# Kernel tuning notes

Measured on AMD Instinct MI355X. Metric: run time of the kernel, lower is better.

Reference implementation:

```python
import jax, jax.numpy as jnp
import numpy as np

N_NODES = 50000
N_EDGES = 800000
IN_F = 128
HID = 256
N_CLS = 10
NUM_GRAPHS = 256


def setup_inputs() -> dict:
    key = jax.random.key(0)
    ks = jax.random.split(key, 8)
    x = jax.random.normal(ks[0], (N_NODES, IN_F), dtype=jnp.float32)
    edge_index = jax.random.randint(ks[1], (2, N_EDGES), 0, N_NODES, dtype=jnp.int64)
    batch = jnp.sort(jax.random.randint(ks[2], (N_NODES,), 0, NUM_GRAPHS, dtype=jnp.int64))
    # Glorot-style init for weights (GCNConv default), zeros bias
    W1 = jax.random.normal(ks[3], (IN_F, HID), dtype=jnp.float32) / np.sqrt(IN_F)
    b1 = jnp.zeros((HID,), dtype=jnp.float32)
    W2 = jax.random.normal(ks[4], (HID, HID), dtype=jnp.float32) / np.sqrt(HID)
    b2 = jnp.zeros((HID,), dtype=jnp.float32)
    Wlin = jax.random.normal(ks[5], (HID, N_CLS), dtype=jnp.float32) / np.sqrt(HID)
    blin = jnp.zeros((N_CLS,), dtype=jnp.float32)
    return {"x": x, "edge_index": edge_index, "batch": batch,
            "W1": W1, "b1": b1, "W2": W2, "b2": b2, "Wlin": Wlin, "blin": blin}


def reference(x, edge_index, batch, W1, b1, W2, b2, Wlin, blin):
    N = x.shape[0]
    # PyG GCNConv default: add self-loops, symmetric normalization D^-1/2 A D^-1/2
    loop = jnp.arange(N, dtype=edge_index.dtype)
    src = jnp.concatenate([edge_index[0], loop])  # message source (row)
    dst = jnp.concatenate([edge_index[1], loop])  # aggregation target (col)
    deg = jax.ops.segment_sum(jnp.ones_like(dst, dtype=x.dtype), dst, num_segments=N)
    dinv = jnp.where(deg > 0, jax.lax.rsqrt(deg), 0.0)
    norm = dinv[src] * dinv[dst]  # [E+N]

    def gcn_conv(h, W, b):
        h = h @ W                          # linear transform first (GCNConv)
        msg = h[src] * norm[:, None]       # gather + edge scale
        agg = jax.ops.segment_sum(msg, dst, num_segments=N)  # scatter-add
        return agg + b

    h = jax.nn.relu(gcn_conv(x, W1, b1))
    h = gcn_conv(h, W2, b2)

    # global_mean_pool over batch ids
    counts = jax.ops.segment_sum(jnp.ones((N,), x.dtype), batch, num_segments=NUM_GRAPHS)
    pooled = jax.ops.segment_sum(h, batch, num_segments=NUM_GRAPHS)
    pooled = pooled / jnp.maximum(counts, 1.0)[:, None]  # [NUM_GRAPHS, HID]

    return pooled @ Wlin + blin  # forward returns logits (softmax unused in forward)
```

## Files before the change

### kernel.cpp

```cpp
#include <hip/hip_runtime.h>
#include <hip/hip_bf16.h>

typedef __hip_bfloat16 bf16;
typedef __attribute__((ext_vector_type(8))) short short8;
typedef __attribute__((ext_vector_type(4))) float f32x4;
typedef __attribute__((ext_vector_type(2))) float f32x2;

#define N_NODES 50000
#define N_EDGES 800000
#define IN_F    128
#define HID     256
#define N_CLS   10
#define N_GRAPH 256

#define NB 98
#define PBLOCKS 256

__device__ __forceinline__ int IG(const int* __restrict__ p, int i, int w) {
    return w ? p[2 * i] : p[i];
}
__device__ __forceinline__ float LF(const void* __restrict__ p, int i, int isbf) {
    return isbf ? __bfloat162float(((const bf16*)p)[i]) : ((const float*)p)[i];
}
__device__ __forceinline__ float b2f(unsigned short h) {
    union { unsigned u; float f; } c; c.u = ((unsigned)h) << 16; return c.f;
}
__device__ __forceinline__ unsigned short f2b(float x) {
    bf16 h = __float2bfloat16(x);
    union { bf16 b; unsigned short u; } c; c.b = h; return c.u;
}
__device__ __forceinline__ float f8s(unsigned b) {
    union { unsigned u; float f; } c;
    c.u = ((b & 0x80u) << 24) | ((b & 0x7Fu) << 20);
    return c.f;
}
#define F8SCALE 0x1p120f
__device__ __forceinline__ unsigned f2fp8(float x) {
    unsigned short h = f2b(x * 0x1p-120f);
    unsigned s = ((unsigned)h >> 8) & 0x80u;
    unsigned mag = (unsigned)h & 0x7FFFu;
    unsigned r = (mag + 7u + ((mag >> 4) & 1u)) >> 4;
    if (r > 0x7Eu) r = 0x7Eu;
    return s | r;
}

#if defined(__has_builtin)
#if __has_builtin(__builtin_amdgcn_cvt_pk_f32_fp8)
#define HW_FP8 1
#endif
#if __has_builtin(__builtin_amdgcn_cvt_pk_fp8_f32)
#define HW_FP8E 1
#endif
#endif

__device__ __forceinline__ f32x2 cvt2lo(unsigned v) {
#ifdef HW_FP8
    return __builtin_amdgcn_cvt_pk_f32_fp8((int)v, false);
#else
    f32x2 r; r[0] = f8s(v & 0xFF) * F8SCALE; r[1] = f8s((v >> 8) & 0xFF) * F8SCALE; return r;
#endif
}
__device__ __forceinline__ f32x2 cvt2hi(unsigned v) {
#ifdef HW_FP8
    return __builtin_amdgcn_cvt_pk_f32_fp8((int)v, true);
#else
    f32x2 r; r[0] = f8s((v >> 16) & 0xFF) * F8SCALE; r[1] = f8s(v >> 24) * F8SCALE; return r;
#endif
}
__device__ __forceinline__ unsigned pk4_fp8(float v0, float v1, float v2, float v3) {
#ifdef HW_FP8E
    int o = __builtin_amdgcn_cvt_pk_fp8_f32(v0, v1, 0, false);
    o = __builtin_amdgcn_cvt_pk_fp8_f32(v2, v3, o, true);
    return (unsigned)o;
#else
    return f2fp8(v0) | (f2fp8(v1) << 8) | (f2fp8(v2) << 16) | (f2fp8(v3) << 24);
#endif
}

__global__ __launch_bounds__(256) void k_detect(const int* __restrict__ ei,
                                                const unsigned short* __restrict__ x,
                                                int* __restrict__ flags) {
    __shared__ int nz, cnt;
    if (threadIdx.x == 0) { nz = 0; cnt = 0; }
    __syncthreads();
    int found = 0, c = 0;
    for (int s = 0; s < 4; ++s) {
        int idx = 2 * (threadIdx.x * 4 + s) + 1;
        if (ei[idx] != 0) found = 1;
    }
    for (int s = 0; s < 8; ++s) {
        unsigned short h = x[threadIdx.x * 8 + s];
        int e = (h >> 7) & 0xFF;
        if (e >= 110 && e <= 135) c++;
    }
    if (found) atomicAdd(&nz, 1);
    atomicAdd(&cnt, c);
    __syncthreads();
    if (threadIdx.x == 0) {
        flags[0] = (nz == 0) ? 1 : 0;
        flags[1] = (cnt > 1536) ? 1 : 0;
    }
}

__global__ __launch_bounds__(256) void k_partA1(const int* __restrict__ ei, int* __restrict__ bucketCnt,
                                                int* __restrict__ blockBase, const int* __restrict__ flags,
                                                int E, int N) {
    __shared__ int h[NB];
    int t = threadIdx.x;
    if (t < NB) h[t] = 0;
    __syncthreads();
    int w = flags[0];
    for (int e = blockIdx.x * 256 + t; e < E; e += PBLOCKS * 256) {
        int d = IG(ei, E + e, w);
        int s = IG(ei, e, w);
        if ((unsigned)d < (unsigned)N && (unsigned)s < (unsigned)N)
            atomicAdd(&h[d >> 9], 1);
    }
    __syncthreads();
    if (t < NB)
        blockBase[blockIdx.x * NB + t] = atomicAdd(&bucketCnt[t * 16], h[t]);
}

__global__ __launch_bounds__(128) void k_bscan(const int* __restrict__ bucketCnt,
                                               int* __restrict__ bucketBase) {
    __shared__ int s[128];
    int t = threadIdx.x;
    int v = (t < NB) ? bucketCnt[t * 16] : 0;
    s[t] = v;
    __syncthreads();
    for (int off = 1; off < 128; off <<= 1) {
        int add = (t >= off) ? s[t - off] : 0;
        __syncthreads();
        s[t] += add;
        __syncthreads();
    }
    if (t <= NB) bucketBase[t] = (t < NB) ? (s[t] - v) : s[NB - 1] + 0;
    if (t == NB - 1) bucketBase[NB] = s[t];
}

__global__ __launch_bounds__(256) void k_partA2(const int* __restrict__ ei,
                                                const int* __restrict__ bucketBase,
                                                const int* __restrict__ blockBase,
                                                unsigned* __restrict__ part,
                                                const int* __restrict__ flags, int E, int N) {
    __shared__ int cur[NB];
    int t = threadIdx.x;
    if (t < NB) cur[t] = bucketBase[t] + blockBase[blockIdx.x * NB + t];
    __syncthreads();
    int w = flags[0];
    for (int e = blockIdx.x * 256 + t; e < E; e += PBLOCKS * 256) {
        int d = IG(ei, E + e, w);
        int s = IG(ei, e, w);
        if ((unsigned)d < (unsigned)N && (unsigned)s < (unsigned)N) {
            int slot = atomicAdd(&cur[d >> 9], 1);
            part[slot] = ((unsigned)(d & 511) << 16) | (unsigned)s;
        }
    }
}

__global__ __launch_bounds__(256) void k_partB(const unsigned* __restrict__ part,
                                               const int* __restrict__ bucketBase,
                                               int* __restrict__ rowptr, float* __restrict__ dinv,
                                               int* __restrict__ col, int N) {
    __shared__ int hist[512];
    __shared__ int scn[512];
    __shared__ int pair[256];
    int b = blockIdx.x, t = threadIdx.x;
    int s0 = bucketBase[b], e0 = bucketBase[b + 1];
    hist[t] = 0; hist[t + 256] = 0;
    __syncthreads();
    for (int j = s0 + t; j < e0; j += 256)
        atomicAdd(&hist[part[j] >> 16], 1);
    __syncthreads();
    int a0 = hist[2 * t], a1 = hist[2 * t + 1];
    int pv = a0 + a1;
    pair[t] = pv;
    __syncthreads();
    for (int off = 1; off < 256; off <<= 1) {
        int add = (t >= off) ? pair[t - off] : 0;
        __syncthreads();
        pair[t] += add;
        __syncthreads();
    }
    int pbase = pair[t] - pv;
    scn[2 * t] = pbase;
    scn[2 * t + 1] = pbase + a0;
    __syncthreads();
#pragma unroll
    for (int hh = 0; hh < 2; ++hh) {
        int l = t + hh * 256;
        int node = b * 512 + l;
        if (node < N) {
            rowptr[node] = s0 + scn[l];
            dinv[node] = rsqrtf((float)(hist[l] + 1));
        }
    }
    if (b == 0 && t == 0) rowptr[N] = bucketBase[NB];
    __syncthreads();
    for (int j = s0 + t; j < e0; j += 256) {
        unsigned p = part[j];
        int pos = s0 + atomicAdd(&scn[p >> 16], 1);
        col[pos] = (int)(p & 0xFFFFu);
    }
}

#define CVTX_BLOCKS 6250
#define CVT1_BLOCKS 128
#define CVT2_BLOCKS 256
#define GB_BLOCKS   196
__global__ __launch_bounds__(256) void k_cvt(const void* __restrict__ x, const float* __restrict__ dinv,
                                             unsigned char* __restrict__ xs8,
                                             const void* __restrict__ W1, unsigned short* __restrict__ w1t,
                                             const void* __restrict__ W2, unsigned short* __restrict__ w2t,
                                             const int* __restrict__ batch, int* __restrict__ gstart,
                                             const int* __restrict__ flags) {
    int b = blockIdx.x;
    int fb = flags[1];
    if (b < CVTX_BLOCKS) {
        int gid = b * 256 + threadIdx.x;
        int row = gid >> 5;
        float d = dinv[row];
        float vx, vy, vz, vw;
        if (fb) {
            ushort4 v = ((const ushort4*)x)[gid];
            vx = b2f(v.x); vy = b2f(v.y); vz = b2f(v.z); vw = b2f(v.w);
        } else {
            float4 v = ((const float4*)x)[gid];
            vx = v.x; vy = v.y; vz = v.z; vw = v.w;
        }
        ((unsigned*)xs8)[gid] = pk4_fp8(vx * d, vy * d, vz * d, vw * d);
    } else if (b < CVTX_BLOCKS + CVT1_BLOCKS) {
        int i = (b - CVTX_BLOCKS) * 256 + threadIdx.x;
        int n = i >> 7, k = i & 127;
        w1t[i] = f2b(LF(W1, k * 256 + n, fb));
    } else if (b < CVTX_BLOCKS + CVT1_BLOCKS + CVT2_BLOCKS) {
        int i = (b - CVTX_BLOCKS - CVT1_BLOCKS) * 256 + threadIdx.x;
        int n = i >> 8, k = i & 255;
        w2t[i] = f2b(LF(W2, k * 256 + n, fb));
    } else {
        int i = (b - CVTX_BLOCKS - CVT1_BLOCKS - CVT2_BLOCKS) * 256 + threadIdx.x;
        if (i <= N_NODES) {
            int w = flags[0];
            int prev = (i == 0) ? -1 : IG(batch, i - 1, w);
            int cur  = (i == N_NODES) ? N_GRAPH : IG(batch, i, w);
            if (prev < -1) prev = -1;
            if (cur > N_GRAPH) cur = N_GRAPH;
            for (int g = prev + 1; g <= cur; ++g)
                if (g >= 0 && g <= N_GRAPH) gstart[g] = i;
        }
    }
}

__global__ __launch_bounds__(256) void k_gemm(const unsigned short* __restrict__ A,
                                              const unsigned short* __restrict__ Bt,
                                              unsigned short* __restrict__ C,
                                              unsigned char* __restrict__ C8, int M, int K,
                                              const float* __restrict__ rowscale,
                                              const void* __restrict__ bias,
                                              const int* __restrict__ flags, int relu) {
    __shared__ unsigned char lds[64 * 132 * 4];
    int t = threadIdx.x;
    int lane = t & 63;
    int w = t >> 6;
    int bm = blockIdx.x * 64;
    int l15 = lane & 15, quad = lane >> 4;

    f32x4 acc[4][4];
#pragma unroll
    for (int ar = 0; ar < 4; ++ar)
#pragma unroll
        for (int tt = 0; tt < 4; ++tt) acc[ar][tt] = (f32x4){0.f, 0.f, 0.f, 0.f};

    const unsigned short* ap[4];
    const unsigned short* bp[4];
#pragma unroll
    for (int ar = 0; ar < 4; ++ar)
        ap[ar] = &A[(size_t)(bm + ar * 16 + l15) * K + quad * 8];
#pragma unroll
    for (int tt = 0; tt < 4; ++tt)
        bp[tt] = &Bt[(size_t)(w * 64 + tt * 16 + l15) * K + quad * 8];

    int nks = K >> 5;
    short8 a[4], b[4];
#pragma unroll
    for (int ar = 0; ar < 4; ++ar) a[ar] = *(const short8*)(ap[ar]);
#pragma unroll
    for (int tt = 0; tt < 4; ++tt) b[tt] = *(const short8*)(bp[tt]);
    for (int ks = 0; ks < nks; ++ks) {
        short8 an[4], bn[4];
        int nxt = (ks + 1) * 32;
        if (ks + 1 < nks) {
#pragma unroll
            for (int ar = 0; ar < 4; ++ar) an[ar] = *(const short8*)(ap[ar] + nxt);
#pragma unroll
            for (int tt = 0; tt < 4; ++tt) bn[tt] = *(const short8*)(bp[tt] + nxt);
        }
#pragma unroll
        for (int ar = 0; ar < 4; ++ar)
#pragma unroll
            for (int tt = 0; tt < 4; ++tt)
                acc[ar][tt] = __builtin_amdgcn_mfma_f32_16x16x32_bf16(b[tt], a[ar], acc[ar][tt], 0, 0, 0);
        if (ks + 1 < nks) {
#pragma unroll
            for (int ar = 0; ar < 4; ++ar) a[ar] = an[ar];
#pragma unroll
            for (int tt = 0; tt < 4; ++tt) b[tt] = bn[tt];
        }
    }

    int fb = flags[1];
    float drow[4];
#pragma unroll
    for (int ar = 0; ar < 4; ++ar) {
        int row = bm + ar * 16 + l15;
        drow[ar] = (rowscale && row < M) ? rowscale[row] : 1.f;
    }
    if (C8) {
        unsigned* Cs = (unsigned*)lds;
#pragma unroll
        for (int tt = 0; tt < 4; ++tt) {
            int colb = w * 64 + tt * 16 + quad * 4;
            float bc[4];
#pragma unroll
            for (int rr = 0; rr < 4; ++rr)
                bc[rr] = bias ? LF(bias, colb + rr, fb) : 0.f;
#pragma unroll
            for (int ar = 0; ar < 4; ++ar) {
                float v[4];
#pragma unroll
                for (int rr = 0; rr < 4; ++rr) {
                    float u = fmaf(acc[ar][tt][rr], drow[ar], bc[rr]);
                    v[rr] = relu ? fmaxf(u, 0.f) : u;
                }
                Cs[(ar * 16 + l15) * 68 + w * 16 + tt * 4 + quad] =
                    pk4_fp8(v[0], v[1], v[2], v[3]);
            }
        }
        __syncthreads();
        int r = t >> 2, h = t & 3;
        if (bm + r < M) {
            const unsigned* src = Cs + r * 68 + h * 16;
            uint4* dst = (uint4*)&C8[(size_t)(bm + r) * 256 + h * 64];
#pragma unroll
            for (int j = 0; j < 4; ++j) dst[j] = *(const uint4*)(src + j * 4);
        }
    } else {
        unsigned short* Cs = (unsigned short*)lds;
#pragma unroll
        for (int tt = 0; tt < 4; ++tt) {
            int colb = w * 64 + tt * 16 + quad * 4;
            float bc[4];
#pragma unroll
            for (int rr = 0; rr < 4; ++rr)
                bc[rr] = bias ? LF(bias, colb + rr, fb) : 0.f;
#pragma unroll
            for (int ar = 0; ar < 4; ++ar) {
                float v[4];
#pragma unroll
                for (int rr = 0; rr < 4; ++rr) {
                    float u = fmaf(acc[ar][tt][rr], drow[ar], bc[rr]);
                    v[rr] = relu ? fmaxf(u, 0.f) : u;
                }
                ushort4 o;
                o.x = f2b(v[0]); o.y = f2b(v[1]); o.z = f2b(v[2]); o.w = f2b(v[3]);
                *(ushort4*)&Cs[(ar * 16 + l15) * 264 + w * 64 + tt * 16 + quad * 4] = o;
            }
        }
        __syncthreads();
        int r = t >> 2, h = t & 3;
        if (bm + r < M) {
            int base = r * 264 + h * 64;
            size_t g = (size_t)(bm + r) * 256 + h * 64;
#pragma unroll
            for (int j = 0; j < 8; ++j)
                *(uint4*)&C[g + j * 8] = *(const uint4*)&Cs[base + j * 8];
        }
    }
}

__global__ __launch_bounds__(256) void k_agg2(const unsigned char* __restrict__ XS,
                                              const int* __restrict__ rowptr, const int* __restrict__ col,
                                              unsigned short* __restrict__ Hout, int N) {
    int lane = threadIdx.x & 63;
    int i = (blockIdx.x * 256 + threadIdx.x) >> 6;
    if (i >= N) return;
    int fo = lane * 2;
    unsigned sv = *(const unsigned short*)&XS[(size_t)i * 128 + fo];
    f32x2 a = cvt2lo(sv);
    int s = rowptr[i], e = rowptr[i + 1];
    int j = s;
    while (j + 16 <= e) {
        unsigned v[16];
#pragma unroll
        for (int q = 0; q < 16; ++q)
            v[q] = *(const unsigned short*)&XS[(size_t)col[j + q] * 128 + fo];
#pragma unroll
        for (int q = 0; q < 16; ++q) a += cvt2lo(v[q]);
        j += 16;
    }
    if (j + 8 <= e) {
        unsigned v[8];
#pragma unroll
        for (int q = 0; q < 8; ++q)
            v[q] = *(const unsigned short*)&XS[(size_t)col[j + q] * 128 + fo];
#pragma unroll
        for (int q = 0; q < 8; ++q) a += cvt2lo(v[q]);
        j += 8;
    }
    if (j + 4 <= e) {
        unsigned v[4];
#pragma unroll
        for (int q = 0; q < 4; ++q)
            v[q] = *(const unsigned short*)&XS[(size_t)col[j + q] * 128 + fo];
#pragma unroll
        for (int q = 0; q < 4; ++q) a += cvt2lo(v[q]);
        j += 4;
    }
    for (; j < e; ++j)
        a += cvt2lo(*(const unsigned short*)&XS[(size_t)col[j] * 128 + fo]);
    ushort2 o;
    o.x = f2b(a[0]); o.y = f2b(a[1]);
    *(ushort2*)&Hout[(size_t)i * 128 + fo] = o;
}

__global__ __launch_bounds__(256) void k_agg4(const unsigned char* __restrict__ XW,
                                              const int* __restrict__ rowptr, const int* __restrict__ col,
                                              const float* __restrict__ dinv, const void* __restrict__ bias,
                                              const int* __restrict__ flags,
                                              unsigned short* __restrict__ Hout, int N) {
    int lane = threadIdx.x & 63;
    int i = (blockIdx.x * 256 + threadIdx.x) >> 6;
    if (i >= N) return;
    int fo = lane * 4;
    unsigned sv = *(const unsigned*)&XW[(size_t)i * 256 + fo];
    f32x2 a01 = cvt2lo(sv), a23 = cvt2hi(sv);
    int s = rowptr[i], e = rowptr[i + 1];
    int j = s;
    while (j + 16 <= e) {
        unsigned v[16];
#pragma unroll
        for (int q = 0; q < 16; ++q)
            v[q] = *(const unsigned*)&XW[(size_t)col[j + q] * 256 + fo];
#pragma unroll
        for (int q = 0; q < 16; ++q) { a01 += cvt2lo(v[q]); a23 += cvt2hi(v[q]); }
        j += 16;
    }
    if (j + 8 <= e) {
        unsigned v[8];
#pragma unroll
        for (int q = 0; q < 8; ++q)
            v[q] = *(const unsigned*)&XW[(size_t)col[j + q] * 256 + fo];
#pragma unroll
        for (int q = 0; q < 8; ++q) { a01 += cvt2lo(v[q]); a23 += cvt2hi(v[q]); }
        j += 8;
    }
    if (j + 4 <= e) {
        unsigned v[4];
#pragma unroll
        for (int q = 0; q < 4; ++q)
            v[q] = *(const unsigned*)&XW[(size_t)col[j + q] * 256 + fo];
#pragma unroll
        for (int q = 0; q < 4; ++q) { a01 += cvt2lo(v[q]); a23 += cvt2hi(v[q]); }
        j += 4;
    }
    for (; j < e; ++j) {
        unsigned v = *(const unsigned*)&XW[(size_t)col[j] * 256 + fo];
        a01 += cvt2lo(v); a23 += cvt2hi(v);
    }
    int fb = flags[1];
    float di = dinv[i];
    float bx = LF(bias, fo + 0, fb), by = LF(bias, fo + 1, fb);
    float bz = LF(bias, fo + 2, fb), bw = LF(bias, fo + 3, fb);
    ushort4 o;
    o.x = f2b(fmaf(a01[0], di, bx)); o.y = f2b(fmaf(a01[1], di, by));
    o.z = f2b(fmaf(a23[0], di, bz)); o.w = f2b(fmaf(a23[1], di, bw));
    *(ushort4*)&Hout[(size_t)i * 256 + fo] = o;
}

__global__ __launch_bounds__(256) void k_poolfinal(const unsigned short* __restrict__ H2,
                                                   const int* __restrict__ gstart,
                                                   const void* __restrict__ Wlin,
                                                   const void* __restrict__ blin,
                                                   const int* __restrict__ flags,
                                                   void* __restrict__ outv) {
    __shared__ float red[4][256];
    __shared__ float p[256];
    int g = blockIdx.x, t = threadIdx.x;
    int sub = t >> 6, lane = t & 63;
    int s = gstart[g], e = gstart[g + 1];
    int cnt = e - s;
    float ax = 0.f, ay = 0.f, az = 0.f, aw = 0.f;
    for (int i = s + sub; i < e; i += 4) {
        ushort4 v = *(const ushort4*)&H2[(size_t)i * 256 + lane * 4];
        ax += b2f(v.x); ay += b2f(v.y); az += b2f(v.z); aw += b2f(v.w);
    }
    red[sub][lane * 4 + 0] = ax;
    red[sub][lane * 4 + 1] = ay;
    red[sub][lane * 4 + 2] = az;
    red[sub][lane * 4 + 3] = aw;
    __syncthreads();
    float inv = 1.f / fmaxf((float)cnt, 1.f);
    p[t] = (red[0][t] + red[1][t] + red[2][t] + red[3][t]) * inv;
    __syncthreads();
    int fb = flags[1];
    if (t < N_CLS) {
        float sum = LF(blin, t, fb);
        for (int f = 0; f < HID; ++f) sum = fmaf(p[f], LF(Wlin, f * N_CLS + t, fb), sum);
        if (fb) ((bf16*)outv)[g * N_CLS + t] = __float2bfloat16(sum);
        else    ((float*)outv)[g * N_CLS + t] = sum;
    }
}

extern "C" void kernel_launch(void* const* d_in, const int* in_sizes, int n_in,
                              void* d_out, int out_size, void* d_ws, size_t ws_size,
                              hipStream_t stream) {
    (void)n_in; (void)ws_size; (void)in_sizes; (void)out_size;
    const void* x     = d_in[0];
    const int*  ei    = (const int*)d_in[1];
    const int*  batch = (const int*)d_in[2];
    const void* W1    = d_in[3];
    const void* b1    = d_in[4];
    const void* W2    = d_in[5];
    const void* b2    = d_in[6];
    const void* Wl    = d_in[7];
    const void* bl    = d_in[8];

    const int N = N_NODES, E = N_EDGES, F = IN_F, H = HID, G = N_GRAPH;

    char* ws = (char*)d_ws;
    size_t off = 0;
    auto alloc = [&](size_t bytes) -> void* {
        void* p = ws + off;
        off += (bytes + 511) & ~(size_t)511;
        return p;
    };
    unsigned char*  xs8  = (unsigned char*)alloc((size_t)N * F);
    unsigned short* aggX = (unsigned short*)alloc((size_t)N * F * 2);
    unsigned short* H1   = (unsigned short*)alloc((size_t)N * H * 2);
    unsigned short* H2   = (unsigned short*)alloc((size_t)N * H * 2);
    unsigned char*  XW2s8 = xs8;
    unsigned short* w1t  = (unsigned short*)alloc((size_t)H * F * 2);
    unsigned short* w2t  = (unsigned short*)alloc((size_t)H * H * 2);
    int*   bucketCnt = (int*)alloc((size_t)NB * 16 * 4);
    int*   bucketBase = (int*)alloc((size_t)(NB + 1) * 4);
    int*   blockBase = (int*)alloc((size_t)PBLOCKS * NB * 4);
    unsigned* part  = (unsigned*)alloc((size_t)E * 4);
    int*   gstart  = (int*)alloc((size_t)(G + 1) * 4);
    float* dinv    = (float*)alloc((size_t)N * 4);
    int*   rowptr  = (int*)alloc((size_t)(N + 1) * 4);
    int*   flags   = (int*)alloc(512);
    int*   col     = (int*)alloc((size_t)E * 4);
    size_t zero_bytes = (size_t)NB * 16 * 4;

    hipMemsetAsync(bucketCnt, 0, zero_bytes, stream);

    k_detect<<<1, 256, 0, stream>>>(ei, (const unsigned short*)x, flags);
    k_partA1<<<PBLOCKS, 256, 0, stream>>>(ei, bucketCnt, blockBase, flags, E, N);
    k_bscan<<<1, 128, 0, stream>>>(bucketCnt, bucketBase);
    k_partA2<<<PBLOCKS, 256, 0, stream>>>(ei, bucketBase, blockBase, part, flags, E, N);
    k_partB<<<NB, 256, 0, stream>>>(part, bucketBase, rowptr, dinv, col, N);

    k_cvt<<<CVTX_BLOCKS + CVT1_BLOCKS + CVT2_BLOCKS + GB_BLOCKS, 256, 0, stream>>>(
        x, dinv, xs8, W1, w1t, W2, w2t, batch, gstart, flags);

    int gemmBlocks = (N + 63) / 64;
    int nbAgg = (N + 3) / 4;

    k_agg2<<<nbAgg, 256, 0, stream>>>(xs8, rowptr, col, aggX, N);
    k_gemm<<<gemmBlocks, 256, 0, stream>>>(aggX, w1t, H1, nullptr, N, F, dinv, b1, flags, 1);
    k_gemm<<<gemmBlocks, 256, 0, stream>>>(H1, w2t, nullptr, XW2s8, N, H, dinv, nullptr, flags, 0);
    k_agg4<<<nbAgg, 256, 0, stream>>>(XW2s8, rowptr, col, dinv, b2, flags, H2, N);
    k_poolfinal<<<G, 256, 0, stream>>>(H2, gstart, Wl, bl, flags, d_out);
}
```

Baseline: 289.8 us.

## Fuse both GCN dense GEMMs into one kernel keeping H1 in LDS

Merges the layer-1 GEMM (with bias, ReLU, dinv scale) and the layer-2 GEMM into one kernel. The 64x256 bf16 H1 tile stays in shared memory instead of making a round trip through global memory. The A tile for GEMM1 is staged in LDS, and the fp8 output now gets its own buffer instead of aliasing xs8. k_agg2's block-to-node mapping is also remapped in an interleaved pattern across eight groups, apparently to spread work across XCDs and improve locality. Larger LDS use (about 51KB) may reduce occupancy.

```diff
diff --git a/kernel.cpp b/kernel.cpp
--- a/kernel.cpp
+++ b/kernel.cpp
@@ -251,19 +251,32 @@
     }
 }
 
-__global__ __launch_bounds__(256) void k_gemm(const unsigned short* __restrict__ A,
-                                              const unsigned short* __restrict__ Bt,
-                                              unsigned short* __restrict__ C,
-                                              unsigned char* __restrict__ C8, int M, int K,
-                                              const float* __restrict__ rowscale,
-                                              const void* __restrict__ bias,
-                                              const int* __restrict__ flags, int relu) {
-    __shared__ unsigned char lds[64 * 132 * 4];
+__global__ __launch_bounds__(256) void k_gcn2l(const unsigned short* __restrict__ A,
+                                               const unsigned short* __restrict__ B1t,
+                                               const unsigned short* __restrict__ B2t,
+                                               unsigned char* __restrict__ C8, int M,
+                                               const float* __restrict__ dinv,
+                                               const void* __restrict__ bias1,
+                                               const int* __restrict__ flags) {
+    __shared__ unsigned short As1[64 * 136];
+    __shared__ unsigned short Hs[64 * 264];
     int t = threadIdx.x;
     int lane = t & 63;
     int w = t >> 6;
     int bm = blockIdx.x * 64;
     int l15 = lane & 15, quad = lane >> 4;
+    int fb = flags[1];
+
+    {
+        const uint4* src = (const uint4*)&A[(size_t)bm * 128];
+#pragma unroll
+        for (int j = 0; j < 4; ++j) {
+            int f = t + j * 256;
+            int row = f >> 4, cu = f & 15;
+            *(uint4*)&As1[row * 136 + cu * 8] = src[(size_t)row * 16 + cu];
+        }
+    }
+    __syncthreads();
 
     f32x4 acc[4][4];
 #pragma unroll
@@ -271,118 +284,95 @@
 #pragma unroll
         for (int tt = 0; tt < 4; ++tt) acc[ar][tt] = (f32x4){0.f, 0.f, 0.f, 0.f};
 
-    const unsigned short* ap[4];
-    const unsigned short* bp[4];
-#pragma unroll
-    for (int ar = 0; ar < 4; ++ar)
-        ap[ar] = &A[(size_t)(bm + ar * 16 + l15) * K + quad * 8];
-#pragma unroll
-    for (int tt = 0; tt < 4; ++tt)
-        bp[tt] = &Bt[(size_t)(w * 64 + tt * 16 + l15) * K + quad * 8];
-
-    int nks = K >> 5;
-    short8 a[4], b[4];
-#pragma unroll
-    for (int ar = 0; ar < 4; ++ar) a[ar] = *(const short8*)(ap[ar]);
-#pragma unroll
-    for (int tt = 0; tt < 4; ++tt) b[tt] = *(const short8*)(bp[tt]);
-    for (int ks = 0; ks < nks; ++ks) {
-        short8 an[4], bn[4];
-        int nxt = (ks + 1) * 32;
-        if (ks + 1 < nks) {
-#pragma unroll
-            for (int ar = 0; ar < 4; ++ar) an[ar] = *(const short8*)(ap[ar] + nxt);
-#pragma unroll
-            for (int tt = 0; tt < 4; ++tt) bn[tt] = *(const short8*)(bp[tt] + nxt);
-        }
+#pragma unroll
+    for (int ks = 0; ks < 4; ++ks) {
+        short8 a[4], b[4];
 #pragma unroll
         for (int ar = 0; ar < 4; ++ar)
-#pragma unroll
-            for (int tt = 0; tt < 4; ++tt)
+            a[ar] = *(const short8*)&As1[(ar * 16 + l15) * 136 + ks * 32 + quad * 8];
+#pragma unroll
+        for (int tt = 0; tt < 4; ++tt)
+            b[tt] = *(const short8*)&B1t[(size_t)(w * 64 + tt * 16 + l15) * 128 + ks * 32 + quad * 8];
+#pragma unroll
+        for (int tt = 0; tt < 4; ++tt)
+#pragma unroll
+            for (int ar = 0; ar < 4; ++ar)
                 acc[ar][tt] = __builtin_amdgcn_mfma_f32_16x16x32_bf16(b[tt], a[ar], acc[ar][tt], 0, 0, 0);
-        if (ks + 1 < nks) {
-#pragma unroll
-            for (int ar = 0; ar < 4; ++ar) a[ar] = an[ar];
-#pragma unroll
-            for (int tt = 0; tt < 4; ++tt) b[tt] = bn[tt];
-        }
-    }
-
-    int fb = flags[1];
+    }
+
     float drow[4];
 #pragma unroll
     for (int ar = 0; ar < 4; ++ar) {
         int row = bm + ar * 16 + l15;
-        drow[ar] = (rowscale && row < M) ? rowscale[row] : 1.f;
-    }
-    if (C8) {
-        unsigned* Cs = (unsigned*)lds;
-#pragma unroll
-        for (int tt = 0; tt < 4; ++tt) {
-            int colb = w * 64 + tt * 16 + quad * 4;
-            float bc[4];
-#pragma unroll
-            for (int rr = 0; rr < 4; ++rr)
-                bc[rr] = bias ? LF(bias, colb + rr, fb) : 0.f;
-#pragma unroll
-            for (int ar = 0; ar < 4; ++ar) {
-                float v[4];
-#pragma unroll
-                for (int rr = 0; rr < 4; ++rr) {
-                    float u = fmaf(acc[ar][tt][rr], drow[ar], bc[rr]);
-                    v[rr] = relu ? fmaxf(u, 0.f) : u;
-                }
-                Cs[(ar * 16 + l15) * 68 + w * 16 + tt * 4 + quad] =
-                    pk4_fp8(v[0], v[1], v[2], v[3]);
-            }
-        }
-        __syncthreads();
-        int r = t >> 2, h = t & 3;
-        if (bm + r < M) {
-            const unsigned* src = Cs + r * 68 + h * 16;
-            uint4* dst = (uint4*)&C8[(size_t)(bm + r) * 256 + h * 64];
-#pragma unroll
-            for (int j = 0; j < 4; ++j) dst[j] = *(const uint4*)(src + j * 4);
-        }
-    } else {
-        unsigned short* Cs = (unsigned short*)lds;
-#pragma unroll
-        for (int tt = 0; tt < 4; ++tt) {
-            int colb = w * 64 + tt * 16 + quad * 4;
-            float bc[4];
-#pragma unroll
-            for (int rr = 0; rr < 4; ++rr)
-                bc[rr] = bias ? LF(bias, colb + rr, fb) : 0.f;
-#pragma unroll
-            for (int ar = 0; ar < 4; ++ar) {
-                float v[4];
-#pragma unroll
-                for (int rr = 0; rr < 4; ++rr) {
-                    float u = fmaf(acc[ar][tt][rr], drow[ar], bc[rr]);
-                    v[rr] = relu ? fmaxf(u, 0.f) : u;
-                }
-                ushort4 o;
-                o.x = f2b(v[0]); o.y = f2b(v[1]); o.z = f2b(v[2]); o.w = f2b(v[3]);
-                *(ushort4*)&Cs[(ar * 16 + l15) * 264 + w * 64 + tt * 16 + quad * 4] = o;
-            }
-        }
-        __syncthreads();
-        int r = t >> 2, h = t & 3;
-        if (bm + r < M) {
-            int base = r * 264 + h * 64;
-            size_t g = (size_t)(bm + r) * 256 + h * 64;
-#pragma unroll
-            for (int j = 0; j < 8; ++j)
-                *(uint4*)&C[g + j * 8] = *(const uint4*)&Cs[base + j * 8];
-        }
+        drow[ar] = (row < M) ? dinv[row] : 1.f;
+    }
+#pragma unroll
+    for (int tt = 0; tt < 4; ++tt) {
+        int colb = w * 64 + tt * 16 + quad * 4;
+        float bc[4];
+#pragma unroll
+        for (int rr = 0; rr < 4; ++rr) bc[rr] = LF(bias1, colb + rr, fb);
+#pragma unroll
+        for (int ar = 0; ar < 4; ++ar) {
+            ushort4 o;
+            o.x = f2b(fmaxf(fmaf(acc[ar][tt][0], drow[ar], bc[0]), 0.f));
+            o.y = f2b(fmaxf(fmaf(acc[ar][tt][1], drow[ar], bc[1]), 0.f));
+            o.z = f2b(fmaxf(fmaf(acc[ar][tt][2], drow[ar], bc[2]), 0.f));
+            o.w = f2b(fmaxf(fmaf(acc[ar][tt][3], drow[ar], bc[3]), 0.f));
+            *(ushort4*)&Hs[(ar * 16 + l15) * 264 + colb] = o;
+            acc[ar][tt] = (f32x4){0.f, 0.f, 0.f, 0.f};
+        }
+    }
+    __syncthreads();
+
+#pragma unroll
+    for (int ks = 0; ks < 8; ++ks) {
+        short8 a[4], b[4];
+#pragma unroll
+        for (int ar = 0; ar < 4; ++ar)
+            a[ar] = *(const short8*)&Hs[(ar * 16 + l15) * 264 + ks * 32 + quad * 8];
+#pragma unroll
+        for (int tt = 0; tt < 4; ++tt)
+            b[tt] = *(const short8*)&B2t[(size_t)(w * 64 + tt * 16 + l15) * 256 + ks * 32 + quad * 8];
+#pragma unroll
+        for (int tt = 0; tt < 4; ++tt)
+#pragma unroll
+            for (int ar = 0; ar < 4; ++ar)
+                acc[ar][tt] = __builtin_amdgcn_mfma_f32_16x16x32_bf16(b[tt], a[ar], acc[ar][tt], 0, 0, 0);
+    }
+
+    unsigned* Cs = (unsigned*)As1;
+    __syncthreads();
+#pragma unroll
+    for (int tt = 0; tt < 4; ++tt) {
+#pragma unroll
+        for (int ar = 0; ar < 4; ++ar) {
+            float v0 = acc[ar][tt][0] * drow[ar];
+            float v1 = acc[ar][tt][1] * drow[ar];
+            float v2 = acc[ar][tt][2] * drow[ar];
+            float v3 = acc[ar][tt][3] * drow[ar];
+            Cs[(ar * 16 + l15) * 68 + w * 16 + tt * 4 + quad] = pk4_fp8(v0, v1, v2, v3);
+        }
+    }
+    __syncthreads();
+    int r = t >> 2, h = t & 3;
+    if (bm + r < M) {
+        const unsigned* src = Cs + r * 68 + h * 16;
+        uint4* dst = (uint4*)&C8[(size_t)(bm + r) * 256 + h * 64];
+#pragma unroll
+        for (int j = 0; j < 4; ++j) dst[j] = *(const uint4*)(src + j * 4);
     }
 }
 
 __global__ __launch_bounds__(256) void k_agg2(const unsigned char* __restrict__ XS,
                                               const int* __restrict__ rowptr, const int* __restrict__ col,
                                               unsigned short* __restrict__ Hout, int N) {
+    int jb = blockIdx.x;
+    int x8 = jb & 7, k = jb >> 3;
+    int gIdx = k >> 4, win = k & 15;
+    int node0 = (gIdx * 8 + x8) * 64 + win * 4;
     int lane = threadIdx.x & 63;
-    int i = (blockIdx.x * 256 + threadIdx.x) >> 6;
+    int i = node0 + (threadIdx.x >> 6);
     if (i >= N) return;
     int fo = lane * 2;
     unsigned sv = *(const unsigned short*)&XS[(size_t)i * 128 + fo];
@@ -536,9 +526,8 @@
     };
     unsigned char*  xs8  = (unsigned char*)alloc((size_t)N * F);
     unsigned short* aggX = (unsigned short*)alloc((size_t)N * F * 2);
-    unsigned short* H1   = (unsigned short*)alloc((size_t)N * H * 2);
+    unsigned char*  XW2s8 = (unsigned char*)alloc((size_t)N * H);
     unsigned short* H2   = (unsigned short*)alloc((size_t)N * H * 2);
-    unsigned char*  XW2s8 = xs8;
     unsigned short* w1t  = (unsigned short*)alloc((size_t)H * F * 2);
     unsigned short* w2t  = (unsigned short*)alloc((size_t)H * H * 2);
     int*   bucketCnt = (int*)alloc((size_t)NB * 16 * 4);
@@ -563,12 +552,12 @@
     k_cvt<<<CVTX_BLOCKS + CVT1_BLOCKS + CVT2_BLOCKS + GB_BLOCKS, 256, 0, stream>>>(
         x, dinv, xs8, W1, w1t, W2, w2t, batch, gstart, flags);
 
-    int gemmBlocks = (N + 63) / 64;
+    int g64 = (N + 63) >> 6;
+    int aggBlocks = ((g64 + 7) >> 3) * 8 * 16;
     int nbAgg = (N + 3) / 4;
 
-    k_agg2<<<nbAgg, 256, 0, stream>>>(xs8, rowptr, col, aggX, N);
-    k_gemm<<<gemmBlocks, 256, 0, stream>>>(aggX, w1t, H1, nullptr, N, F, dinv, b1, flags, 1);
-    k_gemm<<<gemmBlocks, 256, 0, stream>>>(H1, w2t, nullptr, XW2s8, N, H, dinv, nullptr, flags, 0);
+    k_agg2<<<aggBlocks, 256, 0, stream>>>(xs8, rowptr, col, aggX, N);
+    k_gcn2l<<<g64, 256, 0, stream>>>(aggX, w1t, w2t, XW2s8, N, dinv, b1, flags);
     k_agg4<<<nbAgg, 256, 0, stream>>>(XW2s8, rowptr, col, dinv, b2, flags, H2, N);
     k_poolfinal<<<G, 256, 0, stream>>>(H2, gstart, Wl, bl, flags, d_out);
 }
```

Result: faster. 260.2 us (-10.2%).
